# Kernel tuning notes

Measured on AMD Instinct MI355X. Metric: run time of the kernel, lower is better.

Reference implementation:

```python
import jax, jax.numpy as jnp
import numpy as np

NODE_SIZE = 100000
DIM = 512
B = 2048
GAMMA = 3.0
LAMB = 20.0
TAU = 8.0


def setup_inputs() -> dict:
    key = jax.random.key(0)
    k1, k2 = jax.random.split(key)
    pairs = jax.random.randint(k1, (B, 2), 0, NODE_SIZE, dtype=jnp.int64 if jax.config.jax_enable_x64 else jnp.int32)
    emb = jax.random.normal(k2, (NODE_SIZE, DIM), dtype=jnp.float32)
    return {"pairs": pairs, "emb": emb}


def _align_loss(pairs, emb):
    l = pairs[:, 0]
    r = pairs[:, 1]
    l_emb = emb[l]                     # [B, D]
    r_emb = emb[r]                     # [B, D]
    pos_dis = jnp.sum(jnp.square(l_emb - r_emb), axis=-1, keepdims=True)  # [B, 1]

    emb_sq = jnp.sum(jnp.square(emb), axis=1)          # [N]

    def squared_dist(A):
        # ||a||^2 + ||b||^2 - 2 a.b  -> [B, N]
        a_sq = jnp.sum(jnp.square(A), axis=1, keepdims=True)
        return a_sq + emb_sq[None, :] - 2.0 * (A @ emb.T)

    l_neg_dis = squared_dist(l_emb)
    r_neg_dis = squared_dist(r_emb)

    # mask = 1 - one_hot(l) - one_hot(r), built without materializing one-hots
    rows = jnp.arange(B)
    mask = jnp.ones((B, NODE_SIZE), dtype=emb.dtype)
    mask = mask.at[rows, l].add(-1.0)
    mask = mask.at[rows, r].add(-1.0)

    def norm_lse(loss):
        loss = loss * mask
        mu = jax.lax.stop_gradient(jnp.mean(loss, axis=-1, keepdims=True))
        sd = jax.lax.stop_gradient(jnp.std(loss, axis=-1, keepdims=True))  # unbiased=False
        loss = (loss - mu) / sd
        return jax.scipy.special.logsumexp(LAMB * loss + TAU, axis=-1)

    l_loss = norm_lse(pos_dis - l_neg_dis + GAMMA)
    r_loss = norm_lse(pos_dis - r_neg_dis + GAMMA)
    return jnp.mean(l_loss + r_loss)


def reference(pairs, emb):
    return _align_loss(pairs, emb)
```

## Files before the change

kernel.cpp:

```cpp
#include <hip/hip_runtime.h>
#include <stdint.h>

#define NODES   100000
#define NPAD    100096
#define DIM     512
#define NPAIR   2048
#define MROWS   4096
#define NB      782
#define MPAGES  32
#define GAMMA_F 3.0f
#define LAMB_F  20.0f
#define TAU_F   8.0f
#define SHIFT_F 140.0f

#define TM 128
#define TN 128
#define BK 64

typedef __attribute__((ext_vector_type(8))) short          short8;
typedef __attribute__((ext_vector_type(8))) unsigned short ushort8;
typedef __attribute__((ext_vector_type(4))) float          f32x4;


__device__ __forceinline__ unsigned short f2bf(float f) {
    unsigned u = __float_as_uint(f);
    u += 0x7FFFu + ((u >> 16) & 1u);
    return (unsigned short)(u >> 16);
}
__device__ __forceinline__ float bf2f(unsigned short h) {
    return __uint_as_float(((unsigned)h) << 16);
}

__device__ __forceinline__ void gload_lds16(const void* g, void* l) {
    unsigned lofs = (unsigned)__builtin_amdgcn_readfirstlane((unsigned)(uintptr_t)l);
    auto lp = reinterpret_cast<__attribute__((address_space(3))) unsigned*>(lofs);
    auto gp = (const __attribute__((address_space(1))) unsigned*)g;
    __builtin_amdgcn_global_load_lds(gp, lp, 16, 0, 0);
}


__global__ void convert_stats_kernel(const float* __restrict__ emb,
                                     unsigned short* __restrict__ Ebf,
                                     float* __restrict__ esq,
                                     float* __restrict__ Spart,
                                     float* __restrict__ Tpart,
                                     float* __restrict__ E1part,
                                     float* __restrict__ E2part) {
    __shared__ float Sl[4][512];
    __shared__ float Tl[4][512];
    __shared__ float ew[8];
    const int b = blockIdx.x, t = threadIdx.x;
    const int lane = t & 63, wave = t >> 6;
    const int r0 = b * 196;
    float sacc[8], tacc[8];
    #pragma unroll
    for (int k = 0; k < 8; ++k) { sacc[k] = 0.f; tacc[k] = 0.f; }
    float e1 = 0.f, e2 = 0.f;
    for (int i = 0; i < 49; ++i) {
        const int row = r0 + i * 4 + wave;
        if (row >= NPAD) continue;
        const bool real = row < NODES;
        float v[8];
        float ss = 0.f;
        if (real) {
            const float4* p = (const float4*)(emb + (size_t)row * DIM + lane * 8);
            float4 a = p[0], bb = p[1];
            v[0]=a.x; v[1]=a.y; v[2]=a.z; v[3]=a.w;
            v[4]=bb.x; v[5]=bb.y; v[6]=bb.z; v[7]=bb.w;
            #pragma unroll
            for (int k = 0; k < 8; ++k) ss += v[k] * v[k];
        } else {
            #pragma unroll
            for (int k = 0; k < 8; ++k) v[k] = 0.f;
        }
        #pragma unroll
        for (int o = 1; o < 64; o <<= 1) ss += __shfl_xor(ss, o);
        ushort8 o8;
        float vr[8];
        #pragma unroll
        for (int k = 0; k < 8; ++k) { o8[k] = f2bf(v[k]); vr[k] = bf2f(o8[k]); }
        *(ushort8*)(Ebf + (size_t)row * DIM + lane * 8) = o8;
        if (lane == 0) esq[row] = ss;
        if (real) {
            #pragma unroll
            for (int k = 0; k < 8; ++k) { sacc[k] += vr[k]; tacc[k] += ss * vr[k]; }
            if (lane == 0) { e1 += ss; e2 += ss * ss; }
        }
    }
    #pragma unroll
    for (int k = 0; k < 8; ++k) {
        Sl[wave][lane * 8 + k] = sacc[k];
        Tl[wave][lane * 8 + k] = tacc[k];
    }
    if (lane == 0) { ew[wave] = e1; ew[4 + wave] = e2; }
    __syncthreads();
    #pragma unroll
    for (int kk = 0; kk < 2; ++kk) {
        const int d = 2 * t + kk;
        Spart[(size_t)b * 512 + d] = Sl[0][d] + Sl[1][d] + Sl[2][d] + Sl[3][d];
        Tpart[(size_t)b * 512 + d] = Tl[0][d] + Tl[1][d] + Tl[2][d] + Tl[3][d];
    }
    if (t == 0) E1part[b] = ew[0] + ew[1] + ew[2] + ew[3];
    if (t == 1) E2part[b] = ew[4] + ew[5] + ew[6] + ew[7];
}

__global__ void stats_merge_kernel(const float* __restrict__ Spart,
                                   const float* __restrict__ Tpart,
                                   const float* __restrict__ E1part,
                                   const float* __restrict__ E2part,
                                   float* __restrict__ Svec,
                                   float* __restrict__ Tvec,
                                   double* __restrict__ E12) {
    const int t = threadIdx.x;
    if (t < 512) {
        float s = 0.f;
        for (int b = 0; b < 512; ++b) s += Spart[(size_t)b * 512 + t];
        Svec[t] = s;
    } else {
        const int d = t - 512;
        float s = 0.f;
        for (int b = 0; b < 512; ++b) s += Tpart[(size_t)b * 512 + d];
        Tvec[d] = s;
    }
    if (t == 0) { double a = 0.0; for (int b = 0; b < 512; ++b) a += (double)E1part[b]; E12[0] = a; }
    if (t == 1) { double a = 0.0; for (int b = 0; b < 512; ++b) a += (double)E2part[b]; E12[1] = a; }
}

__global__ void gather_kernel(const int* __restrict__ pairs,
                              const float* __restrict__ emb,
                              unsigned short* __restrict__ Abf,
                              float* __restrict__ cvec,
                              float* __restrict__ posv) {
    const int p    = blockIdx.x;
    const int lane = threadIdx.x;
    const int li = pairs[2 * p], ri = pairs[2 * p + 1];
    const float4* pl = (const float4*)(emb + (size_t)li * DIM + lane * 8);
    const float4* pr = (const float4*)(emb + (size_t)ri * DIM + lane * 8);
    float4 a0 = pl[0], a1 = pl[1];
    float4 b0 = pr[0], b1 = pr[1];
    float la[8] = {a0.x,a0.y,a0.z,a0.w,a1.x,a1.y,a1.z,a1.w};
    float lb[8] = {b0.x,b0.y,b0.z,b0.w,b1.x,b1.y,b1.z,b1.w};
    float sa = 0.f, sb = 0.f, sd = 0.f;
    ushort8 oa, ob;
    #pragma unroll
    for (int i = 0; i < 8; ++i) {
        sa += la[i] * la[i];
        sb += lb[i] * lb[i];
        float d = la[i] - lb[i];
        sd += d * d;
        oa[i] = f2bf(la[i]);
        ob[i] = f2bf(lb[i]);
    }
    *(ushort8*)(Abf + (size_t)p * DIM + lane * 8)            = oa;
    *(ushort8*)(Abf + (size_t)(NPAIR + p) * DIM + lane * 8)  = ob;
    #pragma unroll
    for (int off = 1; off < 64; off <<= 1) {
        sa += __shfl_xor(sa, off);
        sb += __shfl_xor(sb, off);
        sd += __shfl_xor(sd, off);
    }
    if (lane == 0) {
        cvec[p]         = sd - sa + GAMMA_F;
        cvec[NPAIR + p] = sd - sb + GAMMA_F;
        posv[p]         = sd;
    }
}


__launch_bounds__(256, 2)
__global__ void gram_kernel(const unsigned short* __restrict__ Ebf,
                            float* __restrict__ Gpart) {
    __shared__ unsigned short ldsA[64 * 128];
    __shared__ unsigned short ldsB[64 * 128];
    const int tid  = threadIdx.x;
    const int lane = tid & 63;
    const int wave = tid >> 6;
    const int wx = wave & 1, wy = wave >> 1;
    const int d1base = blockIdx.y * 128;
    const int d2base = blockIdx.x * 128;
    const int bz = blockIdx.z;
    const int r15 = lane & 15, q = lane >> 4;

    f32x4 zero4 = {0.f, 0.f, 0.f, 0.f};
    f32x4 acc[4][4];
    #pragma unroll
    for (int i = 0; i < 4; ++i)
        #pragma unroll
        for (int j = 0; j < 4; ++j) acc[i][j] = zero4;

    for (int jc = bz; jc < NPAD / 64; jc += 32) {
        const int j0 = jc * 64;
        #pragma unroll
        for (int ii = 0; ii < 4; ++ii) {
            const int iss = wave * 4 + ii;
            const int row = iss * 4 + (lane >> 4);
            gload_lds16(Ebf + (size_t)(j0 + row) * DIM + d1base + (lane & 15) * 8,
                        &ldsA[iss * 4 * 128]);
            gload_lds16(Ebf + (size_t)(j0 + row) * DIM + d2base + (lane & 15) * 8,
                        &ldsB[iss * 4 * 128]);
        }
        __builtin_amdgcn_s_waitcnt(0);
        __syncthreads();
        #pragma unroll
        for (int h = 0; h < 2; ++h) {
            short8 af[4], bfv[4];
            #pragma unroll
            for (int mt = 0; mt < 4; ++mt) {
                const int m = wy * 64 + mt * 16 + r15;
                #pragma unroll
                for (int i = 0; i < 8; ++i)
                    af[mt][i] = (short)ldsA[(h * 32 + q * 8 + i) * 128 + m];
            }
            #pragma unroll
            for (int nt = 0; nt < 4; ++nt) {
                const int n = wx * 64 + nt * 16 + r15;
                #pragma unroll
                for (int i = 0; i < 8; ++i)
                    bfv[nt][i] = (short)ldsB[(h * 32 + q * 8 + i) * 128 + n];
            }
            #pragma unroll
            for (int mt = 0; mt < 4; ++mt)
                #pragma unroll
                for (int nt = 0; nt < 4; ++nt)
                    acc[mt][nt] = __builtin_amdgcn_mfma_f32_16x16x32_bf16(
                        af[mt], bfv[nt], acc[mt][nt], 0, 0, 0);
        }
        __syncthreads();
    }
    float* gp = Gpart + (size_t)bz * 512 * 512;
    #pragma unroll
    for (int mt = 0; mt < 4; ++mt)
        #pragma unroll
        for (int r = 0; r < 4; ++r) {
            const int d1 = d1base + wy * 64 + mt * 16 + q * 4 + r;
            #pragma unroll
            for (int nt = 0; nt < 4; ++nt) {
                const int d2 = d2base + wx * 64 + nt * 16 + r15;
                gp[d1 * 512 + d2] = acc[mt][nt][r];
            }
        }
}

__global__ void gram_merge_kernel(const float* __restrict__ Gpart,
                                  float* __restrict__ G) {
    const int idx = blockIdx.x * 256 + threadIdx.x;
    float s = 0.f;
    for (int b = 0; b < 32; ++b) s += Gpart[(size_t)b * 512 * 512 + idx];
    G[idx] = s;
}


__launch_bounds__(256)
__global__ void gu_kernel(const unsigned short* __restrict__ Abf,
                          const float* __restrict__ G,
                          const float* __restrict__ Svec,
                          const float* __restrict__ Tvec,
                          const double* __restrict__ E12,
                          const float* __restrict__ cvec,
                          const float* __restrict__ posv,
                          const int* __restrict__ pairs,
                          float* __restrict__ alpha_v,
                          float* __restrict__ shift_v) {
    __shared__ float u[8][512];
    __shared__ float red[8][3][4];
    const int t = threadIdx.x;
    const int lane = t & 63, wave = t >> 6;
    const int r0 = blockIdx.x * 8;
    #pragma unroll
    for (int p = 0; p < 8; ++p) {
        unsigned pk = *(const unsigned*)(Abf + (size_t)(r0 + p) * DIM + 2 * t);
        u[p][2 * t]     = bf2f((unsigned short)(pk & 0xffffu));
        u[p][2 * t + 1] = bf2f((unsigned short)(pk >> 16));
    }
    __syncthreads();
    float acc0[8], acc1[8];
    #pragma unroll
    for (int p = 0; p < 8; ++p) { acc0[p] = 0.f; acc1[p] = 0.f; }
    for (int d1 = 0; d1 < 512; ++d1) {
        const float2 g = *(const float2*)(G + d1 * 512 + 2 * t);
        #pragma unroll
        for (int p = 0; p < 8; ++p) {
            const float up = u[p][d1];
            acc0[p] += up * g.x;
            acc1[p] += up * g.y;
        }
    }
    const float sv0 = Svec[2 * t], sv1 = Svec[2 * t + 1];
    const float tv0 = Tvec[2 * t], tv1 = Tvec[2 * t + 1];
    #pragma unroll
    for (int p = 0; p < 8; ++p) {
        const float u0 = u[p][2 * t], u1 = u[p][2 * t + 1];
        float pdS = u0 * sv0 + u1 * sv1;
        float pdT = u0 * tv0 + u1 * tv1;
        float pq  = u0 * acc0[p] + u1 * acc1[p];
        #pragma unroll
        for (int off = 1; off < 64; off <<= 1) {
            pdS += __shfl_xor(pdS, off);
            pdT += __shfl_xor(pdT, off);
            pq  += __shfl_xor(pq,  off);
        }
        if (lane == 0) {
            red[p][0][wave] = pdS;
            red[p][1][wave] = pdT;
            red[p][2][wave] = pq;
        }
    }
    __syncthreads();
    if (t < 8) {
        const int p = t;
        const double dS = (double)red[p][0][0] + red[p][0][1] + red[p][0][2] + red[p][0][3];
        const double dT = (double)red[p][1][0] + red[p][1][1] + red[p][1][2] + red[p][1][3];
        const double qq = (double)red[p][2][0] + red[p][2][1] + red[p][2][2] + red[p][2][3];
        const int row = r0 + p;
        const int pp  = row & (NPAIR - 1);
        const double c  = (double)cvec[row];
        const double E1 = E12[0], E2 = E12[1];
        const double N  = (double)NODES;
        double Sx  = N * c + 2.0 * dS - E1;
        double Sxx = (N * c * c - 2.0 * c * E1 + E2) + 4.0 * (c * dS - dT) + 4.0 * qq;
        const int li = pairs[2 * pp], ri = pairs[2 * pp + 1];
        const double pos = (double)posv[pp];
        if (li != ri) {
            const double x1 = pos + (double)GAMMA_F, x2 = (double)GAMMA_F;
            Sx  -= x1 + x2;
            Sxx -= x1 * x1 + x2 * x2;
        } else {
            Sx -= 2.0 * (double)GAMMA_F;
        }
        const double mu  = Sx / N;
        const double var = Sxx / N - mu * mu;
        const double sd  = sqrt(fmax(var, 1e-30));
        const double al  = (double)LAMB_F / sd;
        alpha_v[row] = (float)al;
        shift_v[row] = (float)(al * mu + (double)SHIFT_F);
    }
}


__launch_bounds__(256, 2)
__global__ void gemm_kernel(const unsigned short* __restrict__ Abf,
                            const unsigned short* __restrict__ Ebf,
                            const float* __restrict__ cvec,
                            const float* __restrict__ esq,
                            const int*   __restrict__ pairs,
                            const float* __restrict__ alpha_v,
                            const float* __restrict__ shift_v,
                            float* __restrict__ psum) {
    __shared__ unsigned short ldsA[TM * BK];
    __shared__ unsigned short ldsB[TN * BK];
    __shared__ float red_s[2][TM];
    __shared__ float alsh[TM], csh[TM], cmsh[TM];
    __shared__ int   lish[TM], rish[TM];

    const int tid  = threadIdx.x;
    const int lane = tid & 63;
    const int wave = tid >> 6;
    const int wx = wave & 1;
    const int wy = wave >> 1;
    const int nb = blockIdx.x;
    const int n0 = nb * TN;
    const int m0 = blockIdx.y * TM;

    if (tid < TM) {
        const int gm = m0 + tid;
        alsh[tid] = alpha_v[gm];
        csh[tid]  = shift_v[gm];
        cmsh[tid] = cvec[gm];
        const int p = gm & (NPAIR - 1);
        lish[tid] = pairs[2 * p];
        rish[tid] = pairs[2 * p + 1];
    }

    f32x4 zero4 = {0.f, 0.f, 0.f, 0.f};
    f32x4 acc[4][4];
    #pragma unroll
    for (int i = 0; i < 4; ++i)
        #pragma unroll
        for (int j = 0; j < 4; ++j) acc[i][j] = zero4;

    const int lrow   = lane >> 3;
    const int lchunk = lane & 7;
    const int r15 = lane & 15;
    const int q   = lane >> 4;

    for (int kt = 0; kt < DIM / BK; ++kt) {
        const int kb = kt * BK;
        #pragma unroll
        for (int j = 0; j < 4; ++j) {
            const int rbase = (wave * 4 + j) * 8;
            const int row   = rbase + lrow;
            const int gch   = lchunk ^ (row & 7);
            gload_lds16(Abf + ((size_t)(m0 + row) * DIM + kb + gch * 8), &ldsA[rbase * BK]);
            gload_lds16(Ebf + ((size_t)(n0 + row) * DIM + kb + gch * 8), &ldsB[rbase * BK]);
        }
        __builtin_amdgcn_s_waitcnt(0);
        __syncthreads();
        #pragma unroll
        for (int h = 0; h < 2; ++h) {
            short8 af[4], bfr[4];
            #pragma unroll
            for (int mt = 0; mt < 4; ++mt) {
                int row = wy * 64 + mt * 16 + r15;
                int c   = (h * 4 + q) ^ (row & 7);
                af[mt] = *(const short8*)&ldsA[row * BK + c * 8];
            }
            #pragma unroll
            for (int nt = 0; nt < 4; ++nt) {
                int row = wx * 64 + nt * 16 + r15;
                int c   = (h * 4 + q) ^ (row & 7);
                bfr[nt] = *(const short8*)&ldsB[row * BK + c * 8];
            }
            #pragma unroll
            for (int mt = 0; mt < 4; ++mt)
                #pragma unroll
                for (int nt = 0; nt < 4; ++nt)
                    acc[mt][nt] = __builtin_amdgcn_mfma_f32_16x16x32_bf16(
                        af[mt], bfr[nt], acc[mt][nt], 0, 0, 0);
        }
        __syncthreads();
    }

    #pragma unroll
    for (int mt = 0; mt < 4; ++mt) {
        #pragma unroll
        for (int r = 0; r < 4; ++r) {
            const int rit = wy * 64 + mt * 16 + q * 4 + r;
            const float cm = cmsh[rit];
            const float al = alsh[rit];
            const float Cc = csh[rit];
            const int li = lish[rit], ri = rish[rit];
            float se = 0.f;
            #pragma unroll
            for (int nt = 0; nt < 4; ++nt) {
                const int gn = n0 + wx * 64 + nt * 16 + r15;
                float xv = cm + 2.0f * acc[mt][nt][r] - esq[gn];
                float msk = 1.0f - (float)(gn == li) - (float)(gn == ri);
                xv *= msk;
                float term = __expf(fmaf(al, xv, -Cc));
                se += (gn < NODES) ? term : 0.f;
            }
            #pragma unroll
            for (int o = 1; o < 16; o <<= 1) se += __shfl_xor(se, o);
            if (r15 == 0) red_s[wx][rit] = se;
        }
    }
    __syncthreads();
    if (tid < TM) {
        psum[(size_t)nb * MROWS + m0 + tid] = red_s[0][tid] + red_s[1][tid];
    }
}


__global__ void lse_part_kernel(const float* __restrict__ psum,
                                float* __restrict__ lsep) {
    const int row = blockIdx.x * 256 + threadIdx.x;
    const int c   = blockIdx.y;
    const int nb0 = c * 196;
    const int nb1 = (nb0 + 196 < NB) ? nb0 + 196 : NB;
    float s = 0.f;
    for (int nb = nb0; nb < nb1; ++nb)
        s += psum[(size_t)nb * MROWS + row];
    lsep[(size_t)c * MROWS + row] = s;
}

__global__ void loss_kernel(const float* __restrict__ lsep,
                            float* __restrict__ loss_v) {
    const int row = blockIdx.x * 256 + threadIdx.x;
    const float s = lsep[row] + lsep[MROWS + row]
                  + lsep[2 * MROWS + row] + lsep[3 * MROWS + row];
    loss_v[row] = (TAU_F + SHIFT_F) + logf(s);
}

__global__ void final_kernel(const float* __restrict__ loss_v,
                             float* __restrict__ out) {
    __shared__ double wpart[4];
    int t = threadIdx.x;
    double s = 0.0;
    for (int i = t; i < MROWS; i += 256)
        s += (double)loss_v[i];
    #pragma unroll
    for (int off = 1; off < 64; off <<= 1) s += __shfl_xor(s, off);
    if ((t & 63) == 0) wpart[t >> 6] = s;
    __syncthreads();
    if (t == 0) out[0] = (float)((wpart[0] + wpart[1] + wpart[2] + wpart[3]) / (double)NPAIR);
}


extern "C" void kernel_launch(void* const* d_in, const int* in_sizes, int n_in,
                              void* d_out, int out_size, void* d_ws, size_t ws_size,
                              hipStream_t stream) {
    const int*   pairs = (const int*)d_in[0];
    const float* emb   = (const float*)d_in[1];
    float* out = (float*)d_out;

    char* ws = (char*)d_ws;
    size_t off = 0;
    auto alloc = [&](size_t bytes) -> void* {
        void* p = ws + off;
        off += (bytes + 255) & ~(size_t)255;
        return p;
    };
    unsigned short* Ebf = (unsigned short*)alloc((size_t)NPAD * DIM * 2);
    unsigned short* Abf = (unsigned short*)alloc((size_t)MROWS * DIM * 2);
    float*  esq     = (float*)alloc((size_t)NPAD * 4);
    float*  cvec    = (float*)alloc((size_t)MROWS * 4);
    float*  posv    = (float*)alloc((size_t)NPAIR * 4);
    float*  Spart   = (float*)alloc((size_t)512 * DIM * 4);
    float*  Tpart   = (float*)alloc((size_t)512 * DIM * 4);
    float*  E1part  = (float*)alloc((size_t)512 * 4);
    float*  E2part  = (float*)alloc((size_t)512 * 4);
    float*  Svec    = (float*)alloc((size_t)DIM * 4);
    float*  Tvec    = (float*)alloc((size_t)DIM * 4);
    double* E12     = (double*)alloc(2 * sizeof(double));
    float*  G       = (float*)alloc((size_t)512 * 512 * 4);
    float*  alpha_v = (float*)alloc((size_t)MROWS * 4);
    float*  shift_v = (float*)alloc((size_t)MROWS * 4);
    float*  lsep    = (float*)alloc((size_t)4 * MROWS * 4);
    float*  loss_v  = (float*)alloc((size_t)MROWS * 4);
    char* uni = (char*)alloc((size_t)32 * 512 * 512 * 4);
    float* Gpart = (float*)uni;
    float* psum  = (float*)uni;
    if (off > ws_size) return;

    convert_stats_kernel<<<512, 256, 0, stream>>>(emb, Ebf, esq,
                                                  Spart, Tpart, E1part, E2part);
    stats_merge_kernel<<<1, 1024, 0, stream>>>(Spart, Tpart, E1part, E2part,
                                               Svec, Tvec, E12);
    gather_kernel<<<NPAIR, 64, 0, stream>>>(pairs, emb, Abf, cvec, posv);

    gram_kernel<<<dim3(4, 4, 32), 256, 0, stream>>>(Ebf, Gpart);
    gram_merge_kernel<<<1024, 256, 0, stream>>>(Gpart, G);
    gu_kernel<<<MROWS / 8, 256, 0, stream>>>(Abf, G, Svec, Tvec, E12,
                                             cvec, posv, pairs, alpha_v, shift_v);

    gemm_kernel<<<dim3(NB, MPAGES), 256, 0, stream>>>(Abf, Ebf, cvec, esq, pairs,
                                                      alpha_v, shift_v, psum);
    lse_part_kernel<<<dim3(16, 4), 256, 0, stream>>>(psum, lsep);
    loss_kernel<<<16, 256, 0, stream>>>(lsep, loss_v);
    final_kernel<<<1, 256, 0, stream>>>(loss_v, out);
}
```

Before: 1.109 ms.

## Enlarge GEMM tiles to 256x256 with double-buffered LDS and interleaved prefetch

The fused distance/exp GEMM moves from 128x128 tiles with 4 waves to 256x256 tiles with 8 waves. It double-buffers LDS so the next K slice loads while MFMAs run, with fine-grained barriers, vmcnt waits and raised wave priority around the MFMA groups. A block-index swizzle groups tiles for L2 reuse, and the esq loads are hoisted out of the epilogue loop. Each block does more reuse per byte loaded but uses more LDS and registers, and the grid shrinks to 391x16 blocks.

Result: no change. 1.126 ms (+1.6%).

```diff
diff --git a/kernel.cpp b/kernel.cpp
--- a/kernel.cpp
+++ b/kernel.cpp
@@ -6,15 +6,15 @@
 #define DIM     512
 #define NPAIR   2048
 #define MROWS   4096
-#define NB      782
-#define MPAGES  32
+#define NBLK    391
+#define MTILES  16
 #define GAMMA_F 3.0f
 #define LAMB_F  20.0f
 #define TAU_F   8.0f
 #define SHIFT_F 140.0f
 
-#define TM 128
-#define TN 128
+#define BM 256
+#define BN 256
 #define BK 64
 
 typedef __attribute__((ext_vector_type(8))) short          short8;
@@ -337,7 +337,53 @@
 }
 
 
-__launch_bounds__(256, 2)
+__device__ __forceinline__ void stage_band(const unsigned short* __restrict__ tile,
+                                           int band, unsigned short* ldsbuf,
+                                           int kb, int lane, int wave) {
+    const int r  = wave * 8 + (lane >> 3);
+    const int ch = (lane & 7) ^ (r & 7);
+    gload_lds16(tile + (size_t)(band * 64 + r) * DIM + kb + ch * 8,
+                ldsbuf + ((size_t)band * 64 + wave * 8) * BK);
+}
+
+template<int H, int MH>
+__device__ __forceinline__ void read_a(const unsigned short* lA, int wr, int r15,
+                                       int q, short8 afr[4]) {
+    #pragma unroll
+    for (int mt4 = 0; mt4 < 4; ++mt4) {
+        const int row = wr * 128 + MH * 64 + mt4 * 16 + r15;
+        const int c   = (H * 4 + q) ^ (row & 7);
+        afr[mt4] = *(const short8*)&lA[row * BK + c * 8];
+    }
+}
+template<int H>
+__device__ __forceinline__ void read_b(const unsigned short* lB, int wc, int r15,
+                                       int q, short8 bfr[4]) {
+    #pragma unroll
+    for (int nt = 0; nt < 4; ++nt) {
+        const int row = wc * 64 + nt * 16 + r15;
+        const int c   = (H * 4 + q) ^ (row & 7);
+        bfr[nt] = *(const short8*)&lB[row * BK + c * 8];
+    }
+}
+template<int MH>
+__device__ __forceinline__ void do_mfma(const short8 afr[4], const short8 bfr[4],
+                                        f32x4 (&acc)[8][4]) {
+    __builtin_amdgcn_s_setprio(1);
+    #pragma unroll
+    for (int mt4 = 0; mt4 < 4; ++mt4)
+        #pragma unroll
+        for (int nt = 0; nt < 4; ++nt)
+            acc[MH * 4 + mt4][nt] = __builtin_amdgcn_mfma_f32_16x16x32_bf16(
+                afr[mt4], bfr[nt], acc[MH * 4 + mt4][nt], 0, 0, 0);
+    __builtin_amdgcn_s_setprio(0);
+}
+
+#define VMCNT2() asm volatile("s_waitcnt vmcnt(2)" ::: "memory")
+#define VMCNT0() asm volatile("s_waitcnt vmcnt(0)" ::: "memory")
+#define SBAR()   __builtin_amdgcn_s_barrier()
+
+__launch_bounds__(512, 2)
 __global__ void gemm_kernel(const unsigned short* __restrict__ Abf,
                             const unsigned short* __restrict__ Ebf,
                             const float* __restrict__ cvec,
@@ -346,22 +392,28 @@
                             const float* __restrict__ alpha_v,
                             const float* __restrict__ shift_v,
                             float* __restrict__ psum) {
-    __shared__ unsigned short ldsA[TM * BK];
-    __shared__ unsigned short ldsB[TN * BK];
-    __shared__ float red_s[2][TM];
-    __shared__ float alsh[TM], csh[TM], cmsh[TM];
-    __shared__ int   lish[TM], rish[TM];
+    __shared__ unsigned short ldsA[2][BM * BK];
+    __shared__ unsigned short ldsB[2][BN * BK];
+    __shared__ float red_s[4][BM];
+    __shared__ float alsh[BM], csh[BM], cmsh[BM];
+    __shared__ int   lish[BM], rish[BM];
 
     const int tid  = threadIdx.x;
     const int lane = tid & 63;
     const int wave = tid >> 6;
-    const int wx = wave & 1;
-    const int wy = wave >> 1;
-    const int nb = blockIdx.x;
-    const int n0 = nb * TN;
-    const int m0 = blockIdx.y * TM;
-
-    if (tid < TM) {
+    const int wr   = wave >> 2;
+    const int wc   = wave & 3;
+    const int r15  = lane & 15;
+    const int q    = lane >> 4;
+
+    const int bid = blockIdx.y * NBLK + blockIdx.x;
+    const int swz = (bid & 7) * 782 + (bid >> 3);
+    const int nb  = swz % NBLK;
+    const int mp  = swz / NBLK;
+    const int n0  = nb * BN;
+    const int m0  = mp * BM;
+
+    if (tid < BM) {
         const int gm = m0 + tid;
         alsh[tid] = alpha_v[gm];
         csh[tid]  = shift_v[gm];
@@ -370,61 +422,102 @@
         lish[tid] = pairs[2 * p];
         rish[tid] = pairs[2 * p + 1];
     }
-
-    f32x4 zero4 = {0.f, 0.f, 0.f, 0.f};
-    f32x4 acc[4][4];
-    #pragma unroll
-    for (int i = 0; i < 4; ++i)
-        #pragma unroll
-        for (int j = 0; j < 4; ++j) acc[i][j] = zero4;
-
-    const int lrow   = lane >> 3;
-    const int lchunk = lane & 7;
-    const int r15 = lane & 15;
-    const int q   = lane >> 4;
-
-    for (int kt = 0; kt < DIM / BK; ++kt) {
-        const int kb = kt * BK;
-        #pragma unroll
-        for (int j = 0; j < 4; ++j) {
-            const int rbase = (wave * 4 + j) * 8;
-            const int row   = rbase + lrow;
-            const int gch   = lchunk ^ (row & 7);
-            gload_lds16(Abf + ((size_t)(m0 + row) * DIM + kb + gch * 8), &ldsA[rbase * BK]);
-            gload_lds16(Ebf + ((size_t)(n0 + row) * DIM + kb + gch * 8), &ldsB[rbase * BK]);
-        }
-        __builtin_amdgcn_s_waitcnt(0);
-        __syncthreads();
-        #pragma unroll
-        for (int h = 0; h < 2; ++h) {
-            short8 af[4], bfr[4];
-            #pragma unroll
-            for (int mt = 0; mt < 4; ++mt) {
-                int row = wy * 64 + mt * 16 + r15;
-                int c   = (h * 4 + q) ^ (row & 7);
-                af[mt] = *(const short8*)&ldsA[row * BK + c * 8];
-            }
-            #pragma unroll
-            for (int nt = 0; nt < 4; ++nt) {
-                int row = wx * 64 + nt * 16 + r15;
-                int c   = (h * 4 + q) ^ (row & 7);
-                bfr[nt] = *(const short8*)&ldsB[row * BK + c * 8];
-            }
-            #pragma unroll
-            for (int mt = 0; mt < 4; ++mt)
-                #pragma unroll
-                for (int nt = 0; nt < 4; ++nt)
-                    acc[mt][nt] = __builtin_amdgcn_mfma_f32_16x16x32_bf16(
-                        af[mt], bfr[nt], acc[mt][nt], 0, 0, 0);
-        }
-        __syncthreads();
-    }
-
-    #pragma unroll
-    for (int mt = 0; mt < 4; ++mt) {
+    __syncthreads();
+
+    const unsigned short* Arow = Abf + (size_t)m0 * DIM;
+    const unsigned short* Brow = Ebf + (size_t)n0 * DIM;
+
+    f32x4 acc[8][4];
+    #pragma unroll
+    for (int i = 0; i < 8; ++i)
+        #pragma unroll
+        for (int j = 0; j < 4; ++j) acc[i][j] = (f32x4){0.f, 0.f, 0.f, 0.f};
+
+    stage_band(Brow, 0, ldsB[0], 0, lane, wave);
+    stage_band(Brow, 1, ldsB[0], 0, lane, wave);
+    stage_band(Brow, 2, ldsB[0], 0, lane, wave);
+    stage_band(Brow, 3, ldsB[0], 0, lane, wave);
+    stage_band(Arow, 0, ldsA[0], 0, lane, wave);
+    stage_band(Arow, 2, ldsA[0], 0, lane, wave);
+    stage_band(Arow, 1, ldsA[0], 0, lane, wave);
+    stage_band(Arow, 3, ldsA[0], 0, lane, wave);
+    VMCNT2();
+    SBAR();
+
+    short8 afr[4], bfr[4];
+
+    for (int kt = 0; kt < 7; ++kt) {
+        unsigned short* lA  = ldsA[kt & 1];
+        unsigned short* lB  = ldsB[kt & 1];
+        unsigned short* lAn = ldsA[(kt & 1) ^ 1];
+        unsigned short* lBn = ldsB[(kt & 1) ^ 1];
+        const int kb2 = (kt + 1) * BK;
+
+        read_a<0, 0>(lA, wr, r15, q, afr);
+        read_b<0>(lB, wc, r15, q, bfr);
+        stage_band(Brow, 0, lBn, kb2, lane, wave);
+        stage_band(Brow, 1, lBn, kb2, lane, wave);
+        SBAR();
+        do_mfma<0>(afr, bfr, acc);
+        VMCNT2();
+        SBAR();
+        read_a<0, 1>(lA, wr, r15, q, afr);
+        stage_band(Brow, 2, lBn, kb2, lane, wave);
+        stage_band(Brow, 3, lBn, kb2, lane, wave);
+        SBAR();
+        do_mfma<1>(afr, bfr, acc);
+        SBAR();
+        read_a<1, 0>(lA, wr, r15, q, afr);
+        read_b<1>(lB, wc, r15, q, bfr);
+        stage_band(Arow, 0, lAn, kb2, lane, wave);
+        stage_band(Arow, 2, lAn, kb2, lane, wave);
+        SBAR();
+        do_mfma<0>(afr, bfr, acc);
+        SBAR();
+        read_a<1, 1>(lA, wr, r15, q, afr);
+        stage_band(Arow, 1, lAn, kb2, lane, wave);
+        stage_band(Arow, 3, lAn, kb2, lane, wave);
+        SBAR();
+        do_mfma<1>(afr, bfr, acc);
+        VMCNT2();
+        SBAR();
+    }
+    {
+        unsigned short* lA = ldsA[1];
+        unsigned short* lB = ldsB[1];
+        read_a<0, 0>(lA, wr, r15, q, afr);
+        read_b<0>(lB, wc, r15, q, bfr);
+        SBAR();
+        do_mfma<0>(afr, bfr, acc);
+        VMCNT0();
+        SBAR();
+        read_a<0, 1>(lA, wr, r15, q, afr);
+        SBAR();
+        do_mfma<1>(afr, bfr, acc);
+        SBAR();
+        read_a<1, 0>(lA, wr, r15, q, afr);
+        read_b<1>(lB, wc, r15, q, bfr);
+        SBAR();
+        do_mfma<0>(afr, bfr, acc);
+        SBAR();
+        read_a<1, 1>(lA, wr, r15, q, afr);
+        SBAR();
+        do_mfma<1>(afr, bfr, acc);
+    }
+
+    float eqv[4];
+    int   gnv[4];
+    #pragma unroll
+    for (int nt = 0; nt < 4; ++nt) {
+        const int gn = n0 + wc * 64 + nt * 16 + r15;
+        gnv[nt] = gn;
+        eqv[nt] = esq[gn];
+    }
+    #pragma unroll
+    for (int mt = 0; mt < 8; ++mt) {
         #pragma unroll
         for (int r = 0; r < 4; ++r) {
-            const int rit = wy * 64 + mt * 16 + q * 4 + r;
+            const int rit = wr * 128 + mt * 16 + q * 4 + r;
             const float cm = cmsh[rit];
             const float al = alsh[rit];
             const float Cc = csh[rit];
@@ -432,21 +525,21 @@
             float se = 0.f;
             #pragma unroll
             for (int nt = 0; nt < 4; ++nt) {
-                const int gn = n0 + wx * 64 + nt * 16 + r15;
-                float xv = cm + 2.0f * acc[mt][nt][r] - esq[gn];
-                float msk = 1.0f - (float)(gn == li) - (float)(gn == ri);
+                float xv = cm + 2.0f * acc[mt][nt][r] - eqv[nt];
+                float msk = 1.0f - (float)(gnv[nt] == li) - (float)(gnv[nt] == ri);
                 xv *= msk;
                 float term = __expf(fmaf(al, xv, -Cc));
-                se += (gn < NODES) ? term : 0.f;
+                se += (gnv[nt] < NODES) ? term : 0.f;
             }
             #pragma unroll
             for (int o = 1; o < 16; o <<= 1) se += __shfl_xor(se, o);
-            if (r15 == 0) red_s[wx][rit] = se;
+            if (r15 == 0) red_s[wc][rit] = se;
         }
     }
     __syncthreads();
-    if (tid < TM) {
-        psum[(size_t)nb * MROWS + m0 + tid] = red_s[0][tid] + red_s[1][tid];
+    if (tid < BM) {
+        psum[(size_t)nb * MROWS + m0 + tid] =
+            red_s[0][tid] + red_s[1][tid] + red_s[2][tid] + red_s[3][tid];
     }
 }
 
@@ -455,8 +548,8 @@
                                 float* __restrict__ lsep) {
     const int row = blockIdx.x * 256 + threadIdx.x;
     const int c   = blockIdx.y;
-    const int nb0 = c * 196;
-    const int nb1 = (nb0 + 196 < NB) ? nb0 + 196 : NB;
+    const int nb0 = c * 98;
+    const int nb1 = (nb0 + 98 < NBLK) ? nb0 + 98 : NBLK;
     float s = 0.f;
     for (int nb = nb0; nb < nb1; ++nb)
         s += psum[(size_t)nb * MROWS + row];
@@ -533,8 +626,8 @@
     gu_kernel<<<MROWS / 8, 256, 0, stream>>>(Abf, G, Svec, Tvec, E12,
                                              cvec, posv, pairs, alpha_v, shift_v);
 
-    gemm_kernel<<<dim3(NB, MPAGES), 256, 0, stream>>>(Abf, Ebf, cvec, esq, pairs,
-                                                      alpha_v, shift_v, psum);
+    gemm_kernel<<<dim3(NBLK, MTILES), 512, 0, stream>>>(Abf, Ebf, cvec, esq, pairs,
+                                                        alpha_v, shift_v, psum);
     lse_part_kernel<<<dim3(16, 4), 256, 0, stream>>>(psum, lsep);
     loss_kernel<<<16, 256, 0, stream>>>(lsep, loss_v);
     final_kernel<<<1, 256, 0, stream>>>(loss_v, out);
```

## Transpose bf16 embeddings so Gram kernel reads K-contiguous swizzled LDS tiles

Applied to the files above, without the earlier changes.

Adds a transpose kernel that writes a [DIM, NPAD] bf16 copy of the embeddings. The Gram (E^T E) kernel then loads K-contiguous rows into LDS with an XOR swizzle and reads MFMA fragments as single 16-byte vector loads, instead of eight strided scalar LDS reads per fragment. The extra pass reads and writes about 100 MB and needs another large workspace buffer, which may offset the gain in the Gram loop.

Result: slower. 1.188 ms (+7.1%).

```diff
diff --git a/kernel.cpp b/kernel.cpp
--- a/kernel.cpp
+++ b/kernel.cpp
@@ -19,6 +19,7 @@
 
 typedef __attribute__((ext_vector_type(8))) short          short8;
 typedef __attribute__((ext_vector_type(8))) unsigned short ushort8;
+typedef __attribute__((ext_vector_type(4))) unsigned short ushort4v;
 typedef __attribute__((ext_vector_type(4))) float          f32x4;
 
 
@@ -167,11 +168,40 @@
 }
 
 
+__global__ void transpose_kernel(const unsigned short* __restrict__ Ebf,
+                                 unsigned short* __restrict__ EbfT) {
+    __shared__ unsigned short tl[64][257];
+    const int t  = threadIdx.x;
+    const int j0 = blockIdx.x * 256;
+    const int d0 = blockIdx.y * 64;
+    const int c  = t & 7;
+    const int rr = t >> 3;
+    #pragma unroll
+    for (int it = 0; it < 8; ++it) {
+        const int r = it * 32 + rr;
+        ushort8 v = *(const ushort8*)(Ebf + (size_t)(j0 + r) * DIM + d0 + c * 8);
+        #pragma unroll
+        for (int i = 0; i < 8; ++i)
+            tl[c * 8 + i][r] = v[i];
+    }
+    __syncthreads();
+    const int lane = t & 63, wave = t >> 6;
+    #pragma unroll
+    for (int it = 0; it < 16; ++it) {
+        const int dd = it * 4 + wave;
+        ushort4v o;
+        #pragma unroll
+        for (int i = 0; i < 4; ++i) o[i] = tl[dd][lane * 4 + i];
+        *(ushort4v*)(EbfT + (size_t)(d0 + dd) * NPAD + j0 + lane * 4) = o;
+    }
+}
+
+
 __launch_bounds__(256, 2)
-__global__ void gram_kernel(const unsigned short* __restrict__ Ebf,
+__global__ void gram_kernel(const unsigned short* __restrict__ EbfT,
                             float* __restrict__ Gpart) {
-    __shared__ unsigned short ldsA[64 * 128];
-    __shared__ unsigned short ldsB[64 * 128];
+    __shared__ unsigned short ldsA[TM * BK];
+    __shared__ unsigned short ldsB[TM * BK];
     const int tid  = threadIdx.x;
     const int lane = tid & 63;
     const int wave = tid >> 6;
@@ -180,6 +210,8 @@
     const int d2base = blockIdx.x * 128;
     const int bz = blockIdx.z;
     const int r15 = lane & 15, q = lane >> 4;
+    const int lrow   = lane >> 3;
+    const int lchunk = lane & 7;
 
     f32x4 zero4 = {0.f, 0.f, 0.f, 0.f};
     f32x4 acc[4][4];
@@ -191,13 +223,14 @@
     for (int jc = bz; jc < NPAD / 64; jc += 32) {
         const int j0 = jc * 64;
         #pragma unroll
-        for (int ii = 0; ii < 4; ++ii) {
-            const int iss = wave * 4 + ii;
-            const int row = iss * 4 + (lane >> 4);
-            gload_lds16(Ebf + (size_t)(j0 + row) * DIM + d1base + (lane & 15) * 8,
-                        &ldsA[iss * 4 * 128]);
-            gload_lds16(Ebf + (size_t)(j0 + row) * DIM + d2base + (lane & 15) * 8,
-                        &ldsB[iss * 4 * 128]);
+        for (int jj = 0; jj < 4; ++jj) {
+            const int rbase = (wave * 4 + jj) * 8;
+            const int row   = rbase + lrow;
+            const int gch   = lchunk ^ (row & 7);
+            gload_lds16(EbfT + ((size_t)(d1base + row) * NPAD + j0 + gch * 8),
+                        &ldsA[rbase * BK]);
+            gload_lds16(EbfT + ((size_t)(d2base + row) * NPAD + j0 + gch * 8),
+                        &ldsB[rbase * BK]);
         }
         __builtin_amdgcn_s_waitcnt(0);
         __syncthreads();
@@ -206,17 +239,15 @@
             short8 af[4], bfv[4];
             #pragma unroll
             for (int mt = 0; mt < 4; ++mt) {
-                const int m = wy * 64 + mt * 16 + r15;
-                #pragma unroll
-                for (int i = 0; i < 8; ++i)
-                    af[mt][i] = (short)ldsA[(h * 32 + q * 8 + i) * 128 + m];
+                const int row = wy * 64 + mt * 16 + r15;
+                const int cc  = (h * 4 + q) ^ (row & 7);
+                af[mt] = *(const short8*)&ldsA[row * BK + cc * 8];
             }
             #pragma unroll
             for (int nt = 0; nt < 4; ++nt) {
-                const int n = wx * 64 + nt * 16 + r15;
-                #pragma unroll
-                for (int i = 0; i < 8; ++i)
-                    bfv[nt][i] = (short)ldsB[(h * 32 + q * 8 + i) * 128 + n];
+                const int row = wx * 64 + nt * 16 + r15;
+                const int cc  = (h * 4 + q) ^ (row & 7);
+                bfv[nt] = *(const short8*)&ldsB[row * BK + cc * 8];
             }
             #pragma unroll
             for (int mt = 0; mt < 4; ++mt)
@@ -500,8 +531,9 @@
         off += (bytes + 255) & ~(size_t)255;
         return p;
     };
-    unsigned short* Ebf = (unsigned short*)alloc((size_t)NPAD * DIM * 2);
-    unsigned short* Abf = (unsigned short*)alloc((size_t)MROWS * DIM * 2);
+    unsigned short* Ebf  = (unsigned short*)alloc((size_t)NPAD * DIM * 2);
+    unsigned short* EbfT = (unsigned short*)alloc((size_t)DIM * NPAD * 2);
+    unsigned short* Abf  = (unsigned short*)alloc((size_t)MROWS * DIM * 2);
     float*  esq     = (float*)alloc((size_t)NPAD * 4);
     float*  cvec    = (float*)alloc((size_t)MROWS * 4);
     float*  posv    = (float*)alloc((size_t)NPAIR * 4);
@@ -528,7 +560,8 @@
                                                Svec, Tvec, E12);
     gather_kernel<<<NPAIR, 64, 0, stream>>>(pairs, emb, Abf, cvec, posv);
 
-    gram_kernel<<<dim3(4, 4, 32), 256, 0, stream>>>(Ebf, Gpart);
+    transpose_kernel<<<dim3(NPAD / 256, DIM / 64), 256, 0, stream>>>(Ebf, EbfT);
+    gram_kernel<<<dim3(4, 4, 32), 256, 0, stream>>>(EbfT, Gpart);
     gram_merge_kernel<<<1024, 256, 0, stream>>>(Gpart, G);
     gu_kernel<<<MROWS / 8, 256, 0, stream>>>(Abf, G, Svec, Tvec, E12,
                                              cvec, posv, pairs, alpha_v, shift_v);
```
